# Kernel tuning notes

Measured on AMD Instinct MI355X. Metric: run time of the kernel, lower is better.

## Reference

```python
import jax, jax.numpy as jnp
import numpy as np

B, CIN, CH, CW = 8192, 3, 7, 7
NHEADS, NODES, D = 3, 49, 64
EPS = 1e-5

def layer_norm(x, axes, gamma=None, beta=None):
    mean = jnp.mean(x, axis=axes, keepdims=True)
    var = jnp.var(x, axis=axes, keepdims=True)
    y = (x - mean) * jax.lax.rsqrt(var + EPS)
    if gamma is not None:
        y = y * gamma + beta
    return y

def setup_inputs() -> dict:
    key = jax.random.key(0)
    ks = iter(jax.random.split(key, 32))
    def w(shape, scale=0.05):
        return (jax.random.normal(next(ks), shape, dtype=jnp.float32) * scale)
    inp = {
        'x': jax.random.normal(next(ks), (B, CIN, CH, CW), dtype=jnp.float32),
        'conv1_w': w((16, 3)), 'conv1_b': w((16,)),
        'conv2_w': w((20, 16)), 'conv2_b': w((20,)),
        'k_proj_w': w((22, NHEADS * D)), 'k_proj_b': w((NHEADS * D,)),
        'q_proj_w': w((22, NHEADS * D)), 'q_proj_b': w((NHEADS * D,)),
        'v_proj_w': w((22, NHEADS * D)), 'v_proj_b': w((NHEADS * D,)),
        'k_norm_g': jnp.ones((NHEADS, NODES, D), jnp.float32), 'k_norm_b': jnp.zeros((NHEADS, NODES, D), jnp.float32),
        'q_norm_g': jnp.ones((NHEADS, NODES, D), jnp.float32), 'q_norm_b': jnp.zeros((NHEADS, NODES, D), jnp.float32),
        'v_norm_g': jnp.ones((NHEADS, NODES, D), jnp.float32), 'v_norm_b': jnp.zeros((NHEADS, NODES, D), jnp.float32),
        'k_lin_w': w((D, NODES)), 'k_lin_b': w((NODES,)),
        'q_lin_w': w((D, NODES)), 'q_lin_b': w((NODES,)),
        'a_lin_w': w((NODES, NODES)), 'a_lin_b': w((NODES,)),
        'lin1_w': w((NHEADS * D, D)), 'lin1_b': w((D,)),
        'lin2_w': w((D, 5)), 'lin2_b': w((5,)),
    }
    return inp

def reference(x, conv1_w, conv1_b, conv2_w, conv2_b,
              k_proj_w, k_proj_b, q_proj_w, q_proj_b, v_proj_w, v_proj_b,
              k_norm_g, k_norm_b, q_norm_g, q_norm_b, v_norm_g, v_norm_b,
              k_lin_w, k_lin_b, q_lin_w, q_lin_b, a_lin_w, a_lin_b,
              lin1_w, lin1_b, lin2_w, lin2_b):
    b = x.shape[0]
    # 1x1 convs == per-pixel linear maps
    h = jax.nn.relu(jnp.einsum('bchw,oc->bohw', x, conv1_w) + conv1_b[None, :, None, None])
    h = jax.nn.relu(jnp.einsum('bchw,oc->bohw', h, conv2_w) + conv2_b[None, :, None, None])
    # spatial coordinate channels, normalized
    xc = jnp.tile((jnp.arange(CW, dtype=x.dtype) / CW)[None, :], (CH, 1))
    yc = jnp.tile((jnp.arange(CH, dtype=x.dtype) / CH)[:, None], (1, CW))
    coords = jnp.broadcast_to(jnp.stack([xc, yc], 0)[None], (b, 2, CH, CW))
    h = jnp.concatenate([h, coords], axis=1)              # [B,22,7,7]
    tokens = h.transpose(0, 2, 3, 1).reshape(b, NODES, -1)  # [B,49,22]

    def proj(w, bias, g, beta):
        p = tokens @ w + bias                              # [B,49,H*D]
        p = p.reshape(b, NODES, NHEADS, D).transpose(0, 2, 1, 3)  # [B,H,N,D]
        return layer_norm(p, (1, 2, 3), g, beta)

    K = proj(k_proj_w, k_proj_b, k_norm_g, k_norm_b)
    Q = proj(q_proj_w, q_proj_b, q_norm_g, q_norm_b)
    V = proj(v_proj_w, v_proj_b, v_norm_g, v_norm_b)

    # additive attention scoring
    A = jax.nn.elu((Q @ q_lin_w + q_lin_b) + (K @ k_lin_w + k_lin_b))  # [B,H,N,N]
    A = A @ a_lin_w + a_lin_b
    A = jax.nn.softmax(A, axis=-1)

    E = jnp.einsum('bhfc,bhcd->bhfd', A, V)                # [B,H,N,D]
    E = E.transpose(0, 2, 1, 3).reshape(b, NODES, NHEADS * D)
    E = jax.nn.relu(E @ lin1_w + lin1_b)                   # [B,N,D]
    E = layer_norm(E, (1, 2))                              # no affine
    E = E.max(axis=1)                                      # [B,D]
    return jax.nn.elu(E @ lin2_w + lin2_b)                 # [B,5]
```

## Files before the change

### kernel.cpp

```cpp
#include <hip/hip_runtime.h>

#define T 512
#define EPS 1e-5f

typedef _Float16 f16x8 __attribute__((ext_vector_type(8)));
typedef _Float16 f16x4 __attribute__((ext_vector_type(4)));
typedef _Float16 f16x2 __attribute__((ext_vector_type(2)));
typedef float f32x4 __attribute__((ext_vector_type(4)));

#define MFMA16(a, b, c) __builtin_amdgcn_mfma_f32_16x16x32_f16((a), (b), (c), 0, 0, 0)
#define SWZ8(row, blk) ((((blk) ^ ((row) & 7)) << 3))

struct Params {
  const float *x;
  const float *c1w, *c1b, *c2w, *c2b;
  const float *kpw, *kpb, *qpw, *qpb, *vpw, *vpb;
  const float *kng, *knb, *qng, *qnb, *vng, *vnb;
  const float *klw, *klb, *qlw, *qlb, *alw, *alb;
  const float *l1w, *l1b, *l2w, *l2b;
  float *out;
};

__global__ __launch_bounds__(256) void prep_weights(Params P, _Float16* ws) {
  int t0 = blockIdx.x * 256 + threadIdx.x;
  int stride = gridDim.x * 256;
  for (int i = t0; i < 3 * 6144; i += stride) {
    int pr = i / 6144, r = i - pr * 6144;
    int j = r >> 5, c = r & 31;
    const float* w = pr == 0 ? P.kpw : pr == 1 ? P.qpw : P.vpw;
    ws[i] = (c < 22) ? (_Float16)w[c * 192 + j] : (_Float16)0.f;
  }
  for (int i = t0; i < 2 * 4096; i += stride) {
    int pr = i >> 12, r = i & 4095;
    int c = r >> 6, d = r & 63;
    const float* w = pr == 0 ? P.qlw : P.klw;
    ws[18432 + i] = (c < 49) ? (_Float16)w[d * 49 + c] : (_Float16)0.f;
  }
  for (int i = t0; i < 4096; i += stride) {
    int c2 = i >> 6, cA = i & 63;
    ws[26624 + i] = (c2 < 49 && cA < 49) ? (_Float16)P.alw[cA * 49 + c2] : (_Float16)0.f;
  }
  for (int i = t0; i < 12288; i += stride) {
    int n = i / 192, k = i - n * 192;
    ws[30720 + i] = (_Float16)P.l1w[k * 64 + n];
  }
  for (int i = t0; i < 2 * 49 * 192; i += stride) {
    int arr = i / 9408, rem = i - arr * 9408;
    int p = rem / 192, j = rem - p * 192;
    int gi = ((j >> 6) * 49 + p) * 64 + (j & 63);
    const float* g  = arr ? P.qng : P.kng;
    const float* bb = arr ? P.qnb : P.knb;
    ws[43008 + i * 2]     = (_Float16)g[gi];
    ws[43008 + i * 2 + 1] = (_Float16)bb[gi];
  }
  for (int i = t0; i < 12288; i += stride) {
    int j = i >> 6, pv = i & 63;
    if (pv < 49) {
      int gi = ((j >> 6) * 49 + pv) * 64 + (j & 63);
      ws[80640 + i * 2]     = (_Float16)P.vng[gi];
      ws[80640 + i * 2 + 1] = (_Float16)P.vnb[gi];
    } else {
      ws[80640 + i * 2]     = (_Float16)0.f;
      ws[80640 + i * 2 + 1] = (_Float16)0.f;
    }
  }
  for (int i = t0; i < 192; i += stride) {
    ws[105216 + i * 2]     = (_Float16)P.kpb[i];
    ws[105216 + i * 2 + 1] = (_Float16)P.qpb[i];
    ws[105600 + i]         = (_Float16)P.vpb[i];
  }
  for (int i = t0; i < 64; i += stride) {
    ws[105792 + i] = (i < 49) ? (_Float16)(P.qlb[i] + P.klb[i]) : (_Float16)0.f;
    ws[105856 + i] = (i < 49) ? (_Float16)P.alb[i] : (_Float16)0.f;
    ws[105920 + i] = (_Float16)P.l1b[i];
  }
}

__device__ inline float elu_f(float v) { return v > 0.f ? v : __expf(v) - 1.f; }

__device__ inline void block_reduce6(float* v, float* sRed, int t) {
  int lane = t & 63, wid = t >> 6;
  #pragma unroll
  for (int k = 0; k < 6; k++) {
    float x = v[k];
    #pragma unroll
    for (int off = 32; off; off >>= 1) x += __shfl_down(x, off, 64);
    if (lane == 0) sRed[k * 8 + wid] = x;
  }
  __syncthreads();
  if (t < 6) {
    float s = 0.f;
    #pragma unroll
    for (int w = 0; w < 8; w++) s += sRed[t * 8 + w];
    sRed[t * 8] = s;
  }
  __syncthreads();
  #pragma unroll
  for (int k = 0; k < 6; k++) v[k] = sRed[k * 8];
}

__device__ inline void block_reduce2(float& sum, float& sq, float* sRed, int t) {
  int lane = t & 63, wid = t >> 6;
  #pragma unroll
  for (int off = 32; off; off >>= 1) {
    sum += __shfl_down(sum, off, 64);
    sq  += __shfl_down(sq,  off, 64);
  }
  if (lane == 0) { sRed[wid] = sum; sRed[8 + wid] = sq; }
  __syncthreads();
  if (t == 0) {
    float s = 0.f, q = 0.f;
    #pragma unroll
    for (int w = 0; w < 8; w++) { s += sRed[w]; q += sRed[8 + w]; }
    sRed[0] = s; sRed[8] = q;
  }
  __syncthreads();
  sum = sRed[0]; sq = sRed[8];
}


__global__ __launch_bounds__(T, 4) void mhr_fused(Params P, const _Float16* __restrict__ ws) {
  const int b = blockIdx.x;
  const int t = threadIdx.x;
  const int wid = t >> 6, l = t & 63, lr = l & 15, lk = l >> 4;

  __shared__ __align__(16) _Float16 sKQ[18816];
  __shared__ __align__(16) _Float16 sA0[9408];
  __shared__ __align__(16) _Float16 sVT[12288];
  __shared__ float sRed[64];
  __shared__ float sM[64];

  _Float16* sTok = sA0;

  for (int i = t; i < 1280; i += T) ((unsigned*)sTok)[i] = 0u;

  float* xb = (float*)sVT;
  float* h1 = (float*)sVT + 160;
  for (int i = t; i < 147; i += T) xb[i] = P.x[b * 147 + i];
  __syncthreads();
  for (int i = t; i < 784; i += T) {
    int p = i >> 4, o = i & 15;
    float a = P.c1b[o] + xb[p] * P.c1w[o * 3] + xb[49 + p] * P.c1w[o * 3 + 1]
            + xb[98 + p] * P.c1w[o * 3 + 2];
    h1[p * 16 + o] = fmaxf(a, 0.f);
  }
  __syncthreads();
  for (int i = t; i < 980; i += T) {
    int p = i / 20, o = i - p * 20;
    float a = P.c2b[o];
    #pragma unroll
    for (int c = 0; c < 16; c++) a += h1[p * 16 + c] * P.c2w[o * 16 + c];
    sTok[p * 40 + o] = (_Float16)fmaxf(a, 0.f);
  }
  for (int i = t; i < 49; i += T) {
    sTok[i * 40 + 20] = (_Float16)((float)(i % 7) * (1.f / 7.f));
    sTok[i * 40 + 21] = (_Float16)((float)(i / 7) * (1.f / 7.f));
  }
  __syncthreads();

  float st[6] = {0.f, 0.f, 0.f, 0.f, 0.f, 0.f};
  #pragma unroll
  for (int i = 0; i < 6; i++) {
    int tt = wid + 8 * i;
    int tm = tt / 12, tn = tt - tm * 12;
    f16x8 a  = *(const f16x8*)&sTok[(tm * 16 + lr) * 40 + lk * 8];
    f16x8 bK = *(const f16x8*)&ws[(tn * 16 + lr) * 32 + lk * 8];
    f16x8 bQ = *(const f16x8*)&ws[6144 + (tn * 16 + lr) * 32 + lk * 8];
    f32x4 z = {0.f, 0.f, 0.f, 0.f};
    f32x4 k4 = MFMA16(a, bK, z);
    f32x4 q4 = MFMA16(a, bQ, z);
    f16x2 b2 = *(const f16x2*)&ws[105216 + (tn * 16 + lr) * 2];
    int j = tn * 16 + lr;
    #pragma unroll
    for (int r = 0; r < 4; r++) {
      int p = tm * 16 + lk * 4 + r;
      float vk = k4[r] + (float)b2.x, vq = q4[r] + (float)b2.y;
      if (p < 49) {
        st[0] += vk; st[1] += vk * vk; st[2] += vq; st[3] += vq * vq;
        int idx = p * 192 + SWZ8(p, j >> 3) + (j & 7);
        sKQ[idx] = (_Float16)vk;
        sKQ[9408 + idx] = (_Float16)vq;
      }
    }
    int vm = tt >> 2, vn = tt & 3;
    f16x8 av = *(const f16x8*)&ws[12288 + (vm * 16 + lr) * 32 + lk * 8];
    f16x8 bt = *(const f16x8*)&sTok[(vn * 16 + lr) * 40 + lk * 8];
    f32x4 v4 = MFMA16(av, bt, z);
    f16x4 vb4 = *(const f16x4*)&ws[105600 + vm * 16 + lk * 4];
    int pv = vn * 16 + lr;
    #pragma unroll
    for (int r = 0; r < 4; r++) {
      int j2 = vm * 16 + lk * 4 + r;
      float vv = v4[r] + (float)vb4[r];
      if (pv < 49) { st[4] += vv; st[5] += vv * vv; }
      sVT[j2 * 64 + SWZ8(j2, pv >> 3) + (pv & 7)] = (_Float16)vv;
    }
  }
  block_reduce6(st, sRed, t);
  float muK = st[0] * (1.f / 9408.f), rrK = rsqrtf(st[1] * (1.f / 9408.f) - muK * muK + EPS);
  float muQ = st[2] * (1.f / 9408.f), rrQ = rsqrtf(st[3] * (1.f / 9408.f) - muQ * muQ + EPS);
  float muV = st[4] * (1.f / 9408.f), rrV = rsqrtf(st[5] * (1.f / 9408.f) - muV * muV + EPS);

  for (int task = t; task < 2352; task += T) {
    int arr = task / 1176, rem = task - arr * 1176;
    int p = rem / 24, blk = rem - p * 24;
    int off = arr * 9408 + p * 192 + SWZ8(p, blk);
    f16x8 raw = *(const f16x8*)&sKQ[off];
    const _Float16* gb = &ws[43008 + ((arr * 49 + p) * 192 + blk * 8) * 2];
    f16x8 g0 = *(const f16x8*)gb;
    f16x8 g1 = *(const f16x8*)(gb + 8);
    float mu = arr ? muQ : muK, rr = arr ? rrQ : rrK;
    f16x8 o8;
    #pragma unroll
    for (int e = 0; e < 8; e++) {
      float g  = (float)(e < 4 ? g0[e * 2]     : g1[(e - 4) * 2]);
      float bb = (float)(e < 4 ? g0[e * 2 + 1] : g1[(e - 4) * 2 + 1]);
      o8[e] = (_Float16)(((float)raw[e] - mu) * rr * g + bb);
    }
    *(f16x8*)&sKQ[off] = o8;
  }
  for (int task = t; task < 1536; task += T) {
    int j = task >> 3, blk = task & 7;
    int off = j * 64 + SWZ8(j, blk);
    f16x8 raw = *(const f16x8*)&sVT[off];
    const _Float16* gb = &ws[80640 + (j * 64 + blk * 8) * 2];
    f16x8 g0 = *(const f16x8*)gb;
    f16x8 g1 = *(const f16x8*)(gb + 8);
    f16x8 o8;
    #pragma unroll
    for (int e = 0; e < 8; e++) {
      float g  = (float)(e < 4 ? g0[e * 2]     : g1[(e - 4) * 2]);
      float bb = (float)(e < 4 ? g0[e * 2 + 1] : g1[(e - 4) * 2 + 1]);
      o8[e] = (_Float16)(((float)raw[e] - muV) * rrV * g + bb);
    }
    *(f16x8*)&sVT[off] = o8;
  }
  __syncthreads();

  #pragma unroll
  for (int i = 0; i < 6; i++) {
    int tt = wid + 8 * i;
    int h = tt >> 4, r16 = tt & 15, tmf = r16 >> 2, tnc = r16 & 3;
    int row = tmf * 16 + lr;
    f32x4 c = {0.f, 0.f, 0.f, 0.f};
    #pragma unroll
    for (int ks = 0; ks < 2; ks++) {
      int ablk = h * 8 + ks * 4 + lk;
      f16x8 aQ = *(const f16x8*)&sKQ[9408 + row * 192 + SWZ8(row, ablk)];
      f16x8 bQ = *(const f16x8*)&ws[18432 + (tnc * 16 + lr) * 64 + ks * 32 + lk * 8];
      c = MFMA16(aQ, bQ, c);
      f16x8 aK = *(const f16x8*)&sKQ[row * 192 + SWZ8(row, ablk)];
      f16x8 bK = *(const f16x8*)&ws[22528 + (tnc * 16 + lr) * 64 + ks * 32 + lk * 8];
      c = MFMA16(aK, bK, c);
    }
    int cc = tnc * 16 + lr;
    float cb = (float)ws[105792 + cc];
    #pragma unroll
    for (int r = 0; r < 4; r++) {
      int f = tmf * 16 + lk * 4 + r;
      if (f < 49)
        sA0[h * 3136 + f * 64 + SWZ8(f, cc >> 3) + (cc & 7)] =
            (cc < 49) ? (_Float16)elu_f(c[r] + cb) : (_Float16)0.f;
    }
  }
  __syncthreads();

  _Float16* A1 = sKQ;
  #pragma unroll
  for (int i = 0; i < 6; i++) {
    int tt = wid + 8 * i;
    int h = tt >> 4, r16 = tt & 15, tmf = r16 >> 2, tnc = r16 & 3;
    int row = tmf * 16 + lr;
    f32x4 c = {0.f, 0.f, 0.f, 0.f};
    #pragma unroll
    for (int ks = 0; ks < 2; ks++) {
      f16x8 a = *(const f16x8*)&sA0[h * 3136 + row * 64 + SWZ8(row, ks * 4 + lk)];
      f16x8 bf = *(const f16x8*)&ws[26624 + (tnc * 16 + lr) * 64 + ks * 32 + lk * 8];
      c = MFMA16(a, bf, c);
    }
    int c2 = tnc * 16 + lr;
    float ab = (float)ws[105856 + c2];
    if (c2 < 49) {
      #pragma unroll
      for (int r = 0; r < 4; r++) {
        int f = tmf * 16 + lk * 4 + r;
        if (f < 49) A1[h * 3136 + f * 64 + SWZ8(f, c2 >> 3) + (c2 & 7)] = (_Float16)(c[r] + ab);
      }
    }
  }
  __syncthreads();

  for (int task = t; task < 1176; task += T) {
    int r_ = task >> 3, cg = task & 7;
    int hh = r_ / 49, f = r_ - hh * 49;
    _Float16* rowp = A1 + hh * 3136 + f * 64;
    float vals[8];
    float mx = -1e30f;
    #pragma unroll
    for (int u = 0; u < 8; u++) {
      int c = cg + u * 8;
      float v = (c < 49) ? (float)rowp[SWZ8(f, u) + cg] : -1e30f;
      vals[u] = v;
      mx = fmaxf(mx, v);
    }
    mx = fmaxf(mx, __shfl_xor(mx, 1, 64));
    mx = fmaxf(mx, __shfl_xor(mx, 2, 64));
    mx = fmaxf(mx, __shfl_xor(mx, 4, 64));
    float s = 0.f;
    #pragma unroll
    for (int u = 0; u < 8; u++) {
      int c = cg + u * 8;
      float e = (c < 49) ? __expf(vals[u] - mx) : 0.f;
      vals[u] = e;
      s += e;
    }
    s += __shfl_xor(s, 1, 64);
    s += __shfl_xor(s, 2, 64);
    s += __shfl_xor(s, 4, 64);
    float inv = 1.f / s;
    #pragma unroll
    for (int u = 0; u < 8; u++) rowp[SWZ8(f, u) + cg] = (_Float16)(vals[u] * inv);
  }
  __syncthreads();

  #pragma unroll
  for (int i = 0; i < 6; i++) {
    int tt = wid + 8 * i;
    int h = tt >> 4, r16 = tt & 15, tmf = r16 >> 2, tnd = r16 & 3;
    int row = tmf * 16 + lr;
    int vrow = h * 64 + tnd * 16 + lr;
    f32x4 c = {0.f, 0.f, 0.f, 0.f};
    #pragma unroll
    for (int ks = 0; ks < 2; ks++) {
      f16x8 a  = *(const f16x8*)&A1[h * 3136 + row * 64 + SWZ8(row, ks * 4 + lk)];
      f16x8 bv = *(const f16x8*)&sVT[vrow * 64 + SWZ8(vrow, ks * 4 + lk)];
      c = MFMA16(a, bv, c);
    }
    int col = h * 64 + tnd * 16 + lr;
    #pragma unroll
    for (int r = 0; r < 4; r++) {
      int f = tmf * 16 + lk * 4 + r;
      if (f < 49) sA0[f * 192 + SWZ8(f, col >> 3) + (col & 7)] = (_Float16)c[r];
    }
  }
  __syncthreads();

  float* F = (float*)sVT;
  float s8 = 0.f, q8 = 0.f;
  #pragma unroll
  for (int i = 0; i < 2; i++) {
    int tile = wid + 8 * i;
    int tmf = tile >> 2, tnn = tile & 3;
    int row = tmf * 16 + lr;
    f32x4 c = {0.f, 0.f, 0.f, 0.f};
    #pragma unroll
    for (int ks = 0; ks < 6; ks++) {
      f16x8 a  = *(const f16x8*)&sA0[row * 192 + SWZ8(row, ks * 4 + lk)];
      f16x8 bf = *(const f16x8*)&ws[30720 + (tnn * 16 + lr) * 192 + ks * 32 + lk * 8];
      c = MFMA16(a, bf, c);
    }
    int n = tnn * 16 + lr;
    float bn = (float)ws[105920 + n];
    #pragma unroll
    for (int r = 0; r < 4; r++) {
      int f = tmf * 16 + lk * 4 + r;
      if (f < 49) {
        float v = fmaxf(c[r] + bn, 0.f);
        F[f * 68 + n] = v;
        s8 += v; q8 += v * v;
      }
    }
  }
  block_reduce2(s8, q8, sRed, t);
  float m8 = s8 * (1.f / 3136.f);
  float r8 = rsqrtf(q8 * (1.f / 3136.f) - m8 * m8 + EPS);
  float* cm = (float*)sA0;
  {
    int d = t & 63, fg = t >> 6;
    float mx = -1e30f;
    #pragma unroll
    for (int u = 0; u < 7; u++) {
      int f = fg * 7 + u;
      if (f < 49) mx = fmaxf(mx, F[f * 68 + d]);
    }
    cm[fg * 64 + d] = mx;
  }
  __syncthreads();
  if (t < 64) {
    float mx = -1e30f;
    #pragma unroll
    for (int g = 0; g < 8; g++) mx = fmaxf(mx, cm[g * 64 + t]);
    sM[t] = (mx - m8) * r8;
  }
  __syncthreads();
  if (t < 320) {
    float v = sM[t & 63] * P.l2w[(t & 63) * 5 + (t >> 6)];
    #pragma unroll
    for (int off = 32; off; off >>= 1) v += __shfl_down(v, off, 64);
    if ((t & 63) == 0) P.out[b * 5 + (t >> 6)] = elu_f(v + P.l2b[t >> 6]);
  }
}

extern "C" void kernel_launch(void* const* d_in, const int* in_sizes, int n_in,
                              void* d_out, int out_size, void* d_ws, size_t ws_size,
                              hipStream_t stream) {
  Params P;
  P.x   = (const float*)d_in[0];
  P.c1w = (const float*)d_in[1];  P.c1b = (const float*)d_in[2];
  P.c2w = (const float*)d_in[3];  P.c2b = (const float*)d_in[4];
  P.kpw = (const float*)d_in[5];  P.kpb = (const float*)d_in[6];
  P.qpw = (const float*)d_in[7];  P.qpb = (const float*)d_in[8];
  P.vpw = (const float*)d_in[9];  P.vpb = (const float*)d_in[10];
  P.kng = (const float*)d_in[11]; P.knb = (const float*)d_in[12];
  P.qng = (const float*)d_in[13]; P.qnb = (const float*)d_in[14];
  P.vng = (const float*)d_in[15]; P.vnb = (const float*)d_in[16];
  P.klw = (const float*)d_in[17]; P.klb = (const float*)d_in[18];
  P.qlw = (const float*)d_in[19]; P.qlb = (const float*)d_in[20];
  P.alw = (const float*)d_in[21]; P.alb = (const float*)d_in[22];
  P.l1w = (const float*)d_in[23]; P.l1b = (const float*)d_in[24];
  P.l2w = (const float*)d_in[25]; P.l2b = (const float*)d_in[26];
  P.out = (float*)d_out;

  _Float16* ws = (_Float16*)d_ws;
  hipLaunchKernelGGL(prep_weights, dim3(64), dim3(256), 0, stream, P, ws);

  int B = in_sizes[0] / 147;
  hipLaunchKernelGGL(mhr_fused, dim3(B), dim3(T), 0, stream, P, ws);
}
```

Before: 413.8 us.

## Swap MFMA operand roles so accumulator rows map to vectorized LDS stores

Every MFMA stage in the fused kernel swaps its A and B operands, so each lane's four accumulator values lie along the contiguous (swizzled) dimension. The scalar half-precision LDS scatter stores become packed 4-wide stores, and the softmax pass reads and writes one 8-wide vector per thread instead of eight strided scalars. Out-of-range rows are clamped to row 48 so the loads stay in bounds. The layernorm apply is also rewritten as two FMAs. This is meant to cut LDS store instruction count and bank traffic, at the cost of extra index arithmetic and some rework of the padding logic.

```diff
diff --git a/kernel.cpp b/kernel.cpp
--- a/kernel.cpp
+++ b/kernel.cpp
@@ -162,39 +162,45 @@
   #pragma unroll
   for (int i = 0; i < 6; i++) {
     int tt = wid + 8 * i;
-    int tm = tt / 12, tn = tt - tm * 12;
-    f16x8 a  = *(const f16x8*)&sTok[(tm * 16 + lr) * 40 + lk * 8];
-    f16x8 bK = *(const f16x8*)&ws[(tn * 16 + lr) * 32 + lk * 8];
-    f16x8 bQ = *(const f16x8*)&ws[6144 + (tn * 16 + lr) * 32 + lk * 8];
+    int jt = tt >> 2, pt = tt & 3;
+    int p = pt * 16 + lr;
+    int j0 = jt * 16 + lk * 4;
+    f16x8 aK = *(const f16x8*)&ws[(jt * 16 + lr) * 32 + lk * 8];
+    f16x8 aQ = *(const f16x8*)&ws[6144 + (jt * 16 + lr) * 32 + lk * 8];
+    f16x8 btok = *(const f16x8*)&sTok[p * 40 + lk * 8];
     f32x4 z = {0.f, 0.f, 0.f, 0.f};
-    f32x4 k4 = MFMA16(a, bK, z);
-    f32x4 q4 = MFMA16(a, bQ, z);
-    f16x2 b2 = *(const f16x2*)&ws[105216 + (tn * 16 + lr) * 2];
-    int j = tn * 16 + lr;
+    f32x4 k4 = MFMA16(aK, btok, z);
+    f32x4 q4 = MFMA16(aQ, btok, z);
+    f16x8 b8 = *(const f16x8*)&ws[105216 + j0 * 2];
+    bool pvld = (p < 49);
+    f16x4 ko, qo;
     #pragma unroll
     for (int r = 0; r < 4; r++) {
-      int p = tm * 16 + lk * 4 + r;
-      float vk = k4[r] + (float)b2.x, vq = q4[r] + (float)b2.y;
-      if (p < 49) {
-        st[0] += vk; st[1] += vk * vk; st[2] += vq; st[3] += vq * vq;
-        int idx = p * 192 + SWZ8(p, j >> 3) + (j & 7);
-        sKQ[idx] = (_Float16)vk;
-        sKQ[9408 + idx] = (_Float16)vq;
-      }
-    }
-    int vm = tt >> 2, vn = tt & 3;
-    f16x8 av = *(const f16x8*)&ws[12288 + (vm * 16 + lr) * 32 + lk * 8];
-    f16x8 bt = *(const f16x8*)&sTok[(vn * 16 + lr) * 40 + lk * 8];
-    f32x4 v4 = MFMA16(av, bt, z);
-    f16x4 vb4 = *(const f16x4*)&ws[105600 + vm * 16 + lk * 4];
-    int pv = vn * 16 + lr;
+      float vk = k4[r] + (float)b8[2 * r];
+      float vq = q4[r] + (float)b8[2 * r + 1];
+      if (pvld) { st[0] += vk; st[1] += vk * vk; st[2] += vq; st[3] += vq * vq; }
+      ko[r] = (_Float16)vk; qo[r] = (_Float16)vq;
+    }
+    if (pvld) {
+      int idx = p * 192 + SWZ8(p, j0 >> 3) + (j0 & 7);
+      *(f16x4*)&sKQ[idx] = ko;
+      *(f16x4*)&sKQ[9408 + idx] = qo;
+    }
+    int pt2 = tt / 12, jt2 = tt - pt2 * 12;
+    int j = jt2 * 16 + lr;
+    int p0 = pt2 * 16 + lk * 4;
+    f16x8 atok = *(const f16x8*)&sTok[(pt2 * 16 + lr) * 40 + lk * 8];
+    f16x8 bV = *(const f16x8*)&ws[12288 + j * 32 + lk * 8];
+    f32x4 v4 = MFMA16(atok, bV, z);
+    float bj = (float)ws[105600 + j];
+    f16x4 vo;
     #pragma unroll
     for (int r = 0; r < 4; r++) {
-      int j2 = vm * 16 + lk * 4 + r;
-      float vv = v4[r] + (float)vb4[r];
-      if (pv < 49) { st[4] += vv; st[5] += vv * vv; }
-      sVT[j2 * 64 + SWZ8(j2, pv >> 3) + (pv & 7)] = (_Float16)vv;
-    }
+      float vv = v4[r] + bj;
+      if (p0 + r < 49) { st[4] += vv; st[5] += vv * vv; }
+      vo[r] = (_Float16)vv;
+    }
+    *(f16x4*)&sVT[j * 64 + SWZ8(j, p0 >> 3) + (p0 & 7)] = vo;
   }
   block_reduce6(st, sRed, t);
   float muK = st[0] * (1.f / 9408.f), rrK = rsqrtf(st[1] * (1.f / 9408.f) - muK * muK + EPS);
@@ -215,7 +221,8 @@
     for (int e = 0; e < 8; e++) {
       float g  = (float)(e < 4 ? g0[e * 2]     : g1[(e - 4) * 2]);
       float bb = (float)(e < 4 ? g0[e * 2 + 1] : g1[(e - 4) * 2 + 1]);
-      o8[e] = (_Float16)(((float)raw[e] - mu) * rr * g + bb);
+      float s  = rr * g;
+      o8[e] = (_Float16)(fmaf((float)raw[e], s, fmaf(-mu, s, bb)));
     }
     *(f16x8*)&sKQ[off] = o8;
   }
@@ -231,7 +238,8 @@
     for (int e = 0; e < 8; e++) {
       float g  = (float)(e < 4 ? g0[e * 2]     : g1[(e - 4) * 2]);
       float bb = (float)(e < 4 ? g0[e * 2 + 1] : g1[(e - 4) * 2 + 1]);
-      o8[e] = (_Float16)(((float)raw[e] - muV) * rrV * g + bb);
+      float s  = rrV * g;
+      o8[e] = (_Float16)(fmaf((float)raw[e], s, fmaf(-muV, s, bb)));
     }
     *(f16x8*)&sVT[off] = o8;
   }
@@ -240,27 +248,27 @@
   #pragma unroll
   for (int i = 0; i < 6; i++) {
     int tt = wid + 8 * i;
-    int h = tt >> 4, r16 = tt & 15, tmf = r16 >> 2, tnc = r16 & 3;
-    int row = tmf * 16 + lr;
+    int h = tt >> 4, r16 = tt & 15, tc = r16 >> 2, tf = r16 & 3;
+    int f = tf * 16 + lr;
+    int rowB = f < 49 ? f : 48;
+    int c0 = tc * 16 + lk * 4;
     f32x4 c = {0.f, 0.f, 0.f, 0.f};
     #pragma unroll
     for (int ks = 0; ks < 2; ks++) {
-      int ablk = h * 8 + ks * 4 + lk;
-      f16x8 aQ = *(const f16x8*)&sKQ[9408 + row * 192 + SWZ8(row, ablk)];
-      f16x8 bQ = *(const f16x8*)&ws[18432 + (tnc * 16 + lr) * 64 + ks * 32 + lk * 8];
+      int kblk = h * 8 + ks * 4 + lk;
+      f16x8 bQ = *(const f16x8*)&sKQ[9408 + rowB * 192 + SWZ8(rowB, kblk)];
+      f16x8 aQ = *(const f16x8*)&ws[18432 + (tc * 16 + lr) * 64 + ks * 32 + lk * 8];
       c = MFMA16(aQ, bQ, c);
-      f16x8 aK = *(const f16x8*)&sKQ[row * 192 + SWZ8(row, ablk)];
-      f16x8 bK = *(const f16x8*)&ws[22528 + (tnc * 16 + lr) * 64 + ks * 32 + lk * 8];
+      f16x8 bK = *(const f16x8*)&sKQ[rowB * 192 + SWZ8(rowB, kblk)];
+      f16x8 aK = *(const f16x8*)&ws[22528 + (tc * 16 + lr) * 64 + ks * 32 + lk * 8];
       c = MFMA16(aK, bK, c);
     }
-    int cc = tnc * 16 + lr;
-    float cb = (float)ws[105792 + cc];
-    #pragma unroll
-    for (int r = 0; r < 4; r++) {
-      int f = tmf * 16 + lk * 4 + r;
-      if (f < 49)
-        sA0[h * 3136 + f * 64 + SWZ8(f, cc >> 3) + (cc & 7)] =
-            (cc < 49) ? (_Float16)elu_f(c[r] + cb) : (_Float16)0.f;
+    f16x4 cb4 = *(const f16x4*)&ws[105792 + c0];
+    if (f < 49) {
+      f16x4 o;
+      #pragma unroll
+      for (int r = 0; r < 4; r++) o[r] = (_Float16)elu_f(c[r] + (float)cb4[r]);
+      *(f16x4*)&sA0[h * 3136 + f * 64 + SWZ8(f, c0 >> 3) + (c0 & 7)] = o;
     }
   }
   __syncthreads();
@@ -269,23 +277,23 @@
   #pragma unroll
   for (int i = 0; i < 6; i++) {
     int tt = wid + 8 * i;
-    int h = tt >> 4, r16 = tt & 15, tmf = r16 >> 2, tnc = r16 & 3;
-    int row = tmf * 16 + lr;
+    int h = tt >> 4, r16 = tt & 15, tc = r16 >> 2, tf = r16 & 3;
+    int f = tf * 16 + lr;
+    int rowB = f < 49 ? f : 48;
+    int c0 = tc * 16 + lk * 4;
     f32x4 c = {0.f, 0.f, 0.f, 0.f};
     #pragma unroll
     for (int ks = 0; ks < 2; ks++) {
-      f16x8 a = *(const f16x8*)&sA0[h * 3136 + row * 64 + SWZ8(row, ks * 4 + lk)];
-      f16x8 bf = *(const f16x8*)&ws[26624 + (tnc * 16 + lr) * 64 + ks * 32 + lk * 8];
-      c = MFMA16(a, bf, c);
-    }
-    int c2 = tnc * 16 + lr;
-    float ab = (float)ws[105856 + c2];
-    if (c2 < 49) {
+      f16x8 bA = *(const f16x8*)&sA0[h * 3136 + rowB * 64 + SWZ8(rowB, ks * 4 + lk)];
+      f16x8 aA = *(const f16x8*)&ws[26624 + (tc * 16 + lr) * 64 + ks * 32 + lk * 8];
+      c = MFMA16(aA, bA, c);
+    }
+    f16x4 ab4 = *(const f16x4*)&ws[105856 + c0];
+    if (f < 49) {
+      f16x4 o;
       #pragma unroll
-      for (int r = 0; r < 4; r++) {
-        int f = tmf * 16 + lk * 4 + r;
-        if (f < 49) A1[h * 3136 + f * 64 + SWZ8(f, c2 >> 3) + (c2 & 7)] = (_Float16)(c[r] + ab);
-      }
+      for (int r = 0; r < 4; r++) o[r] = (_Float16)(c[r] + (float)ab4[r]);
+      *(f16x4*)&A1[h * 3136 + f * 64 + SWZ8(f, c0 >> 3) + (c0 & 7)] = o;
     }
   }
   __syncthreads();
@@ -293,14 +301,15 @@
   for (int task = t; task < 1176; task += T) {
     int r_ = task >> 3, cg = task & 7;
     int hh = r_ / 49, f = r_ - hh * 49;
-    _Float16* rowp = A1 + hh * 3136 + f * 64;
+    int off = hh * 3136 + f * 64 + SWZ8(f, cg);
+    f16x8 raw = *(const f16x8*)&A1[off];
+    int nv = cg < 6 ? 8 : (cg == 6 ? 1 : 0);
     float vals[8];
     float mx = -1e30f;
     #pragma unroll
-    for (int u = 0; u < 8; u++) {
-      int c = cg + u * 8;
-      float v = (c < 49) ? (float)rowp[SWZ8(f, u) + cg] : -1e30f;
-      vals[u] = v;
+    for (int e = 0; e < 8; e++) {
+      float v = (e < nv) ? (float)raw[e] : -1e30f;
+      vals[e] = v;
       mx = fmaxf(mx, v);
     }
     mx = fmaxf(mx, __shfl_xor(mx, 1, 64));
@@ -308,39 +317,42 @@
     mx = fmaxf(mx, __shfl_xor(mx, 4, 64));
     float s = 0.f;
     #pragma unroll
-    for (int u = 0; u < 8; u++) {
-      int c = cg + u * 8;
-      float e = (c < 49) ? __expf(vals[u] - mx) : 0.f;
-      vals[u] = e;
-      s += e;
+    for (int e = 0; e < 8; e++) {
+      float ex = (e < nv) ? __expf(vals[e] - mx) : 0.f;
+      vals[e] = ex;
+      s += ex;
     }
     s += __shfl_xor(s, 1, 64);
     s += __shfl_xor(s, 2, 64);
     s += __shfl_xor(s, 4, 64);
     float inv = 1.f / s;
-    #pragma unroll
-    for (int u = 0; u < 8; u++) rowp[SWZ8(f, u) + cg] = (_Float16)(vals[u] * inv);
+    f16x8 o8;
+    #pragma unroll
+    for (int e = 0; e < 8; e++) o8[e] = (_Float16)(vals[e] * inv);
+    *(f16x8*)&A1[off] = o8;
   }
   __syncthreads();
 
   #pragma unroll
   for (int i = 0; i < 6; i++) {
     int tt = wid + 8 * i;
-    int h = tt >> 4, r16 = tt & 15, tmf = r16 >> 2, tnd = r16 & 3;
-    int row = tmf * 16 + lr;
-    int vrow = h * 64 + tnd * 16 + lr;
+    int h = tt >> 4, r16 = tt & 15, td = r16 >> 2, tf = r16 & 3;
+    int f = tf * 16 + lr;
+    int rowB = f < 49 ? f : 48;
+    int vrow = h * 64 + td * 16 + lr;
+    int j0 = h * 64 + td * 16 + lk * 4;
     f32x4 c = {0.f, 0.f, 0.f, 0.f};
     #pragma unroll
     for (int ks = 0; ks < 2; ks++) {
-      f16x8 a  = *(const f16x8*)&A1[h * 3136 + row * 64 + SWZ8(row, ks * 4 + lk)];
-      f16x8 bv = *(const f16x8*)&sVT[vrow * 64 + SWZ8(vrow, ks * 4 + lk)];
-      c = MFMA16(a, bv, c);
-    }
-    int col = h * 64 + tnd * 16 + lr;
-    #pragma unroll
-    for (int r = 0; r < 4; r++) {
-      int f = tmf * 16 + lk * 4 + r;
-      if (f < 49) sA0[f * 192 + SWZ8(f, col >> 3) + (col & 7)] = (_Float16)c[r];
+      f16x8 aV = *(const f16x8*)&sVT[vrow * 64 + SWZ8(vrow, ks * 4 + lk)];
+      f16x8 bA = *(const f16x8*)&A1[h * 3136 + rowB * 64 + SWZ8(rowB, ks * 4 + lk)];
+      c = MFMA16(aV, bA, c);
+    }
+    if (f < 49) {
+      f16x4 o;
+      #pragma unroll
+      for (int r = 0; r < 4; r++) o[r] = (_Float16)c[r];
+      *(f16x4*)&sA0[f * 192 + SWZ8(f, j0 >> 3) + (j0 & 7)] = o;
     }
   }
   __syncthreads();
@@ -350,25 +362,27 @@
   #pragma unroll
   for (int i = 0; i < 2; i++) {
     int tile = wid + 8 * i;
-    int tmf = tile >> 2, tnn = tile & 3;
-    int row = tmf * 16 + lr;
+    int tn_ = tile >> 2, tf = tile & 3;
+    int f = tf * 16 + lr;
+    int rowB = f < 49 ? f : 48;
+    int n0 = tn_ * 16 + lk * 4;
     f32x4 c = {0.f, 0.f, 0.f, 0.f};
     #pragma unroll
     for (int ks = 0; ks < 6; ks++) {
-      f16x8 a  = *(const f16x8*)&sA0[row * 192 + SWZ8(row, ks * 4 + lk)];
-      f16x8 bf = *(const f16x8*)&ws[30720 + (tnn * 16 + lr) * 192 + ks * 32 + lk * 8];
-      c = MFMA16(a, bf, c);
-    }
-    int n = tnn * 16 + lr;
-    float bn = (float)ws[105920 + n];
-    #pragma unroll
-    for (int r = 0; r < 4; r++) {
-      int f = tmf * 16 + lk * 4 + r;
-      if (f < 49) {
-        float v = fmaxf(c[r] + bn, 0.f);
-        F[f * 68 + n] = v;
+      f16x8 aL = *(const f16x8*)&ws[30720 + (tn_ * 16 + lr) * 192 + ks * 32 + lk * 8];
+      f16x8 bE = *(const f16x8*)&sA0[rowB * 192 + SWZ8(rowB, ks * 4 + lk)];
+      c = MFMA16(aL, bE, c);
+    }
+    f16x4 bn4 = *(const f16x4*)&ws[105920 + n0];
+    if (f < 49) {
+      f32x4 o;
+      #pragma unroll
+      for (int r = 0; r < 4; r++) {
+        float v = fmaxf(c[r] + (float)bn4[r], 0.f);
+        o[r] = v;
         s8 += v; q8 += v * v;
       }
+      *(f32x4*)&F[f * 68 + n0] = o;
     }
   }
   block_reduce2(s8, q8, sRed, t);
```

Measured after the change: 605.7 us. 1.46x slower.
